# Kernel tuning notes

Measured on AMD Instinct MI355X. Metric: run time of the kernel, lower is better.

Reference implementation:

```python
import jax, jax.numpy as jnp
import numpy as np


def _gru_dir(x, Wih, Whh, bih, bhh):
    # x: (B,T,I) -> (B,T,H); torch GRU equations, h0 = 0
    H = Whh.shape[1]
    pre = x @ Wih.T + bih  # (B,T,3H), input projection hoisted out of scan
    def step(h, p):
        gh = h @ Whh.T + bhh
        pr, pz, pn = jnp.split(p, 3, axis=-1)
        gr, gz, gn = jnp.split(gh, 3, axis=-1)
        r = jax.nn.sigmoid(pr + gr)
        z = jax.nn.sigmoid(pz + gz)
        n = jnp.tanh(pn + r * gn)
        h = (1.0 - z) * n + z * h
        return h, h
    h0 = jnp.zeros((x.shape[0], H), x.dtype)
    _, ys = jax.lax.scan(step, h0, jnp.swapaxes(pre, 0, 1))
    return jnp.swapaxes(ys, 0, 1)


def _gru_bidir(x, Wih, Whh, bih, bhh):
    f = _gru_dir(x, Wih[0], Whh[0], bih[0], bhh[0])
    b = _gru_dir(x[:, ::-1], Wih[1], Whh[1], bih[1], bhh[1])[:, ::-1]
    return jnp.concatenate([f, b], axis=-1)


def _forward(inputs, embed, l_Wih, l_Whh, l_bih, l_bhh, r_Wih, r_Whh, r_bih, r_bhh,
             a_Wih, a_Whh, a_bih, a_bhh, Wc1, Wc2, vc, Wb, Wd, vd, Wm, vm, Ws, vs,
             Wp, vp, Wpred):
    x = embed[inputs]  # (B,T,E)
    hl = _gru_bidir(x, l_Wih, l_Whh, l_bih, l_bhh)  # (B,T,2H)
    hr = _gru_bidir(x, r_Wih, r_Whh, r_bih, r_bhh)  # (B,T,2H)
    # co-attention: score[b,i,j] = vc . tanh(Wc1 hl_j + Wc2 hr_i)
    s = jnp.tanh((hl @ Wc1.T)[:, None, :, :] + (hr @ Wc2.T)[:, :, None, :])  # (B,T,T,H)
    ptc = jax.nn.softmax((s @ vc.T)[..., 0], axis=-1) @ hl
    # bilinear: hr (Wb hl)^T
    sjt = jnp.einsum('bid,bjd->bij', hr, hl @ Wb.T)
    ptb = jax.nn.softmax(sjt, axis=-1) @ hl
    # multiplicative: vd . tanh(Wd (hl_j * hr_i))
    p = hl[:, None, :, :] * hr[:, :, None, :]  # (B,T,T,2H)
    ptd = jax.nn.softmax((jnp.tanh(p @ Wd.T) @ vd.T)[..., 0], axis=-1) @ hl
    # subtractive: vm . tanh(Wm (hl_j - hr_i))
    d = hl[:, None, :, :] - hr[:, :, None, :]  # (B,T,T,2H)
    ptm = jax.nn.softmax((jnp.tanh(d @ Wm.T) @ vm.T)[..., 0], axis=-1) @ hl
    # self-attention on hr: vs . tanh(Ws (hr_j * hr_i))
    ss = hr[:, None, :, :] * hr[:, :, None, :]  # (B,T,T,2H)
    pts = jax.nn.softmax((jnp.tanh(ss @ Ws.T) @ vs.T)[..., 0], axis=-1) @ hr
    agg = jnp.concatenate([hr, pts, ptc, ptd, ptb, ptm], axis=-1)  # (B,T,12H)
    ar = _gru_bidir(agg, a_Wih, a_Whh, a_bih, a_bhh)  # (B,T,2H)
    # pooling of hl
    sj = jax.nn.softmax(jnp.swapaxes(jnp.tanh(hl @ Wp.T) @ vp.T, 1, 2), axis=-1)  # (B,1,T)
    rl = sj @ hl  # (B,1,2H)
    # final attention over aggregation
    sj2 = jax.nn.softmax(jnp.swapaxes((ar @ Wc1.T + rl @ Wc2.T) @ vc.T, 1, 2), axis=-1)  # (B,1,T)
    rr = (sj2 @ ar)[:, 0, :]  # (B,2H)
    return jax.nn.sigmoid(rr @ Wpred.T)  # (B,labels)


def setup_inputs() -> dict:
    B, T, V, E, H, L = 4, 256, 30000, 300, 128, 2
    key = jax.random.key(0)
    ks = jax.random.split(key, 40)
    inp = {}
    inp['inputs'] = jax.random.randint(ks[0], (B, T), 0, V)
    inp['embed'] = jax.random.uniform(ks[1], (V, E), jnp.float32, -0.1, 0.1)
    ki = 2
    for name, isz in [('l', E), ('r', E), ('a', 12 * H)]:
        inp[name + '_Wih'] = jax.random.normal(ks[ki], (2, 3 * H, isz), jnp.float32) * 0.05; ki += 1
        inp[name + '_Whh'] = jax.random.normal(ks[ki], (2, 3 * H, H), jnp.float32) * 0.05; ki += 1
        inp[name + '_bih'] = jnp.zeros((2, 3 * H), jnp.float32)
        inp[name + '_bhh'] = jnp.zeros((2, 3 * H), jnp.float32)
    for n, o, i in [('Wc1', H, 2 * H), ('Wc2', H, 2 * H), ('vc', 1, H), ('Wb', 2 * H, 2 * H),
                    ('Wd', H, 2 * H), ('vd', 1, H), ('Wm', H, 2 * H), ('vm', 1, H),
                    ('Ws', H, 2 * H), ('vs', 1, H), ('Wp', H, 2 * H), ('vp', 1, H),
                    ('Wpred', L, 2 * H)]:
        inp[n] = jax.random.normal(ks[ki], (o, i), jnp.float32) * 0.05; ki += 1
    return inp


def reference(inputs, embed, l_Wih, l_Whh, l_bih, l_bhh, r_Wih, r_Whh, r_bih, r_bhh,
              a_Wih, a_Whh, a_bih, a_bhh, Wc1, Wc2, vc, Wb, Wd, vd, Wm, vm, Ws, vs,
              Wp, vp, Wpred):
    return _forward(inputs, embed, l_Wih, l_Whh, l_bih, l_bhh, r_Wih, r_Whh, r_bih,
                    r_bhh, a_Wih, a_Whh, a_bih, a_bhh, Wc1, Wc2, vc, Wb, Wd, vd, Wm,
                    vm, Ws, vs, Wp, vp, Wpred)
```

## Files before the change

kernel.cpp:

```cpp
#include <hip/hip_runtime.h>


#define DEV static __device__ __forceinline__
#define BAR_LGKM() __asm__ volatile("s_waitcnt lgkmcnt(0)\ns_barrier" ::: "memory")

typedef __attribute__((ext_vector_type(4))) float f32x4;
typedef __attribute__((ext_vector_type(8))) short s16x8;
typedef __attribute__((ext_vector_type(4))) unsigned int u32x4;

constexpr int T = 256, E = 300, EP = 320, H = 128, H2 = 256, H3 = 384, H12 = 1536;
constexpr int M = 1024;
constexpr int STY = 262144;

DEV float b2f(unsigned short h) { return __uint_as_float(((unsigned)h) << 16); }
DEV unsigned short f2b(float f) {
  unsigned u = __float_as_uint(f);
  u += 0x7fff + ((u >> 16) & 1);
  return (unsigned short)(u >> 16);
}
DEV unsigned cvt_pk_bf16(float lo, float hi) {
  unsigned r;
  __asm__("v_cvt_pk_bf16_f32 %0, %1, %2" : "=v"(r) : "v"(lo), "v"(hi));
  return r;
}
DEV float rcp_f(float x) {
  float r;
  __asm__("v_rcp_f32 %0, %1" : "=v"(r) : "v"(x));
  return r;
}
DEV float sigm(float x) { return rcp_f(1.f + __expf(-x)); }
DEV float tanh_f(float x) {
  float e = __expf(2.f * x);
  return __builtin_fmaf(-2.f, rcp_f(e + 1.f), 1.f);
}

DEV s16x8 ldfrag(const unsigned short* p) {
  u32x4 v = *(const u32x4*)p;
  return __builtin_bit_cast(s16x8, v);
}
DEV f32x4 mfma16(s16x8 a, s16x8 b, f32x4 c) {
  return __builtin_amdgcn_mfma_f32_16x16x32_bf16(a, b, c, 0, 0, 0);
}


struct StageArgs {
  const float* cs[9]; unsigned short* cd[9]; int cn[9];
  const int* idx; const float* emb; unsigned short* xhi; unsigned short* xlo;
  const float* lW; const float* rW; unsigned short* wpad;
};

__global__ void k_stage(StageArgs sa) {
  int seg = blockIdx.y;
  int i = blockIdx.x * 256 + threadIdx.x;
  if (seg < 9) {
    if (i < sa.cn[seg]) sa.cd[seg][i] = f2b(sa.cs[seg][i]);
    return;
  }
  if (seg == 9) {
    if (i >= M * EP) return;
    int m = i / EP, e = i - m * EP;
    int r = sa.idx[m];
    float v = (e < E) ? sa.emb[(size_t)r * E + e] : 0.f;
    unsigned short hi = f2b(v);
    sa.xhi[i] = hi;
    sa.xlo[i] = f2b(v - b2f(hi));
    return;
  }
  if (i >= 4 * H3 * EP) return;
  int e = i % EP, n = (i / EP) % H3, uu = i / (EP * H3);
  const float* src = (uu < 2 ? sa.lW : sa.rW) + (size_t)((uu & 1) * H3 + n) * E;
  sa.wpad[i] = (e < E) ? f2b(src[e]) : (unsigned short)0;
}


struct GemmDesc {
  const unsigned short* Ahi; const unsigned short* Alo; const unsigned short* W;
  const float* bias; float* Cf; int N; int K; int tr;
};
struct GemmBatch { GemmDesc d[8]; };

__global__ __launch_bounds__(256) void k_gemm(GemmBatch gb) {
  GemmDesc g = gb.d[blockIdx.z];
  int nb = blockIdx.y * 64;
  if (nb >= g.N) return;
  int mb = blockIdx.x * 64;
  int lane = threadIdx.x & 63, w = threadIdx.x >> 6, quad = lane >> 4, l16 = lane & 15;
  int K = g.K;
  const unsigned short* Ahp = g.Ahi + (size_t)(mb + w * 16 + l16) * K + quad * 8;
  const unsigned short* Alp = g.Alo + (size_t)(mb + w * 16 + l16) * K + quad * 8;
  const unsigned short* Wp = g.W + (size_t)(nb + l16) * K + quad * 8;
  f32x4 acc[4];
  #pragma unroll
  for (int nt = 0; nt < 4; ++nt) acc[nt] = f32x4{0.f, 0.f, 0.f, 0.f};
  for (int k = 0; k < K; k += 32) {
    s16x8 ah = ldfrag(Ahp + k);
    s16x8 al = ldfrag(Alp + k);
    #pragma unroll
    for (int nt = 0; nt < 4; ++nt) {
      s16x8 b = ldfrag(Wp + (size_t)nt * 16 * K + k);
      acc[nt] = mfma16(ah, b, acc[nt]);
      acc[nt] = mfma16(al, b, acc[nt]);
    }
  }
  int mr0 = mb + w * 16 + quad * 4;
  #pragma unroll
  for (int nt = 0; nt < 4; ++nt) {
    int col = nb + nt * 16 + l16;
    float bv = g.bias ? g.bias[col] : 0.f;
    #pragma unroll
    for (int r = 0; r < 4; ++r) {
      if (g.tr)
        g.Cf[(size_t)col * M + (mr0 + r)] = acc[nt][r] + bv;
      else
        g.Cf[(size_t)(mr0 + r) * g.N + col] = acc[nt][r] + bv;
    }
  }
}


struct RecArgs {
  const unsigned short* whh[4];
  const float* pre[4];
  float* outf[4];
  unsigned short* outhi[4];
  unsigned short* outlo[4];
  unsigned short* agghi[4];
  unsigned short* agglo[4];
  const float* bhh[4];
  int colOff[4];
  int dir[4];
};

__global__ __launch_bounds__(512) void k_gru(RecArgs ra) {
  int u = blockIdx.x;
  __shared__ __align__(16) unsigned short hs[2][16 * 136];
  int tid = threadIdx.x, lane = tid & 63, w8 = tid >> 6;
  int quad = lane >> 4, l16 = lane & 15;
  for (int i = tid; i < 2 * 16 * 136; i += 512) ((unsigned short*)hs)[i] = 0;
  const unsigned short* whh = ra.whh[u];
  s16x8 bq[3][4];
  #pragma unroll
  for (int g = 0; g < 3; ++g) {
    int row = g * 128 + w8 * 16 + l16;
    #pragma unroll
    for (int kc = 0; kc < 4; ++kc)
      bq[g][kc] = ldfrag(whh + (size_t)row * H + kc * 32 + quad * 8);
  }
  const float* bhh = ra.bhh[u];
  const float* pre = ra.pre[u];
  float* outf = ra.outf[u];
  unsigned short* outhi = ra.outhi[u];
  unsigned short* outlo = ra.outlo[u];
  unsigned short* agghi = ra.agghi[u];
  unsigned short* agglo = ra.agglo[u];
  int colOff = ra.colOff[u], dir = ra.dir[u];
  int b = ((quad & 1) << 1) | (quad >> 1);
  int d = w8 * 16 + l16;
  float bh_r = bhh[d], bh_z = bhh[d + 128], bh_n = bhh[d + 256];
  float hf = 0.f;
  float ob[8];
  unsigned short obh[8], obl[8];
  int t0 = dir ? (T - 1) : 0;
  const float* pq = pre + (size_t)(b * T + t0) * H3 + d;
  float n_pr = pq[0], n_pz = pq[128], n_pn = pq[256];
  long pst = dir ? -(long)H3 : (long)H3;
  __syncthreads();
  for (int sb = 0; sb < T; sb += 8) {
    #pragma unroll
    for (int ss = 0; ss < 8; ++ss) {
      float pr = n_pr, pz = n_pz, pn = n_pn;
      pq += pst;
      n_pr = pq[0]; n_pz = pq[128]; n_pn = pq[256];
      const unsigned short* hcur = hs[ss & 1];
      unsigned short* hnxt = hs[(ss & 1) ^ 1];
      s16x8 ah[4];
      #pragma unroll
      for (int kc = 0; kc < 4; ++kc)
        ah[kc] = ldfrag(hcur + l16 * 136 + kc * 32 + quad * 8);
      f32x4 accA[3], accB[3];
      #pragma unroll
      for (int g = 0; g < 3; ++g) {
        accA[g] = f32x4{0.f, 0.f, 0.f, 0.f};
        accB[g] = f32x4{0.f, 0.f, 0.f, 0.f};
      }
      #pragma unroll
      for (int g = 0; g < 3; ++g) accA[g] = mfma16(ah[0], bq[g][0], accA[g]);
      #pragma unroll
      for (int g = 0; g < 3; ++g) accB[g] = mfma16(ah[2], bq[g][2], accB[g]);
      #pragma unroll
      for (int g = 0; g < 3; ++g) accA[g] = mfma16(ah[1], bq[g][1], accA[g]);
      #pragma unroll
      for (int g = 0; g < 3; ++g) accB[g] = mfma16(ah[3], bq[g][3], accB[g]);
      float ghv[3];
      #pragma unroll
      for (int g = 0; g < 3; ++g) {
        float x0 = (accA[g][0] + accB[g][0]) + (accA[g][1] + accB[g][1]);
        float x1 = (accA[g][2] + accB[g][2]) + (accA[g][3] + accB[g][3]);
        float y1 = __shfl_xor(x1, 32);
        ghv[g] = (quad >= 2) ? y1 : x0;
      }
      float rg = sigm(pr + ghv[0] + bh_r);
      float zg = sigm(pz + ghv[1] + bh_z);
      float ng = tanh_f(pn + rg * (ghv[2] + bh_n));
      hf = (1.f - zg) * ng + zg * hf;
      unsigned short hi = f2b(hf);
      unsigned short lo = f2b(hf - b2f(hi));
      hnxt[(2 * b) * 136 + d] = hi;
      hnxt[(2 * b + 1) * 136 + d] = lo;
      ob[ss] = hf; obh[ss] = hi; obl[ss] = lo;
      BAR_LGKM();
    }
    #pragma unroll
    for (int qq = 0; qq < 8; ++qq) {
      int sq = sb + qq;
      int tq = dir ? (T - 1 - sq) : sq;
      size_t o = (size_t)(b * T + tq) * H2 + colOff + d;
      outf[o] = ob[qq]; outhi[o] = obh[qq]; outlo[o] = obl[qq];
      if (agghi) {
        size_t a = (size_t)(b * T + tq) * H12 + colOff + d;
        agghi[a] = obh[qq]; agglo[a] = obl[qq];
      }
    }
  }
}


struct ScArgs {
  const unsigned short* Xhi[2];
  const float* Rf; const float* Wt[2]; const float* vt[2];
  float* So[2]; float* So2[2];
  const float *Hc, *Rc, *Hm, *Rm, *HB, *hrf, *vcf, *vmf; float* S;
};

__global__ __launch_bounds__(256, 2) void k_score(ScArgs a) {
  __shared__ __align__(16) unsigned char smem[32768];
  int which = blockIdx.y;
  int bi = blockIdx.x;
  int tid = threadIdx.x;
  if (which == 4) {
    if (bi >= 128) return;
    int b = bi >> 5, i0 = (bi & 31) << 3;
    int gi0 = b * 256 + i0;
    float* rc_l = (float*)smem;
    float* rm_l = rc_l + 1024;
    float* hr_l = rm_l + 1024;
    float* vc_l = hr_l + 2048;
    float* vm_l = vc_l + 128;
    {
      const float4* rc4 = (const float4*)(a.Rc + (size_t)gi0 * 128);
      const float4* rm4 = (const float4*)(a.Rm + (size_t)gi0 * 128);
      ((float4*)rc_l)[tid] = rc4[tid];
      ((float4*)rm_l)[tid] = rm4[tid];
      const float4* hr4 = (const float4*)(a.hrf + (size_t)gi0 * 256);
      ((float4*)hr_l)[tid] = hr4[tid];
      ((float4*)hr_l)[256 + tid] = hr4[256 + tid];
      if (tid < 128) { vc_l[tid] = a.vcf[tid]; vm_l[tid] = a.vmf[tid]; }
    }
    __syncthreads();
    int j = tid;
    size_t cb = (size_t)(b * 256 + j);
    float scq[8], smq[8], sbq[8];
    #pragma unroll
    for (int q = 0; q < 8; ++q) { scq[q] = 0.f; smq[q] = 0.f; sbq[q] = 0.f; }
    for (int k = 0; k < 128; ++k) {
      float hc = a.Hc[(size_t)k * M + cb];
      float hm = a.Hm[(size_t)k * M + cb];
      float vck = vc_l[k], vmk = vm_l[k];
      #pragma unroll
      for (int q = 0; q < 8; ++q) {
        scq[q] += vck * tanh_f(hc + rc_l[q * 128 + k]);
        smq[q] += vmk * tanh_f(hm - rm_l[q * 128 + k]);
      }
    }
    for (int k = 0; k < 256; ++k) {
      float hb = a.HB[(size_t)k * M + cb];
      #pragma unroll
      for (int q = 0; q < 8; ++q) sbq[q] += hb * hr_l[q * 256 + k];
    }
    #pragma unroll
    for (int q = 0; q < 8; ++q) {
      size_t o = (size_t)(gi0 + q) * 256 + j;
      a.S[(size_t)STY * 1 + o] = scq[q];
      a.S[(size_t)STY * 3 + o] = sbq[q];
      a.S[(size_t)STY * 4 + o] = smq[q];
    }
    return;
  }
  int type = which >> 1, khb = which & 1;
  int b = bi >> 8;
  const unsigned short* Xhi = a.Xhi[type];
  const float* W = a.Wt[type] + (size_t)khb * 64 * 256;
  const float* v = a.vt[type] + khb * 64;
  float* Sout = khb ? a.So2[type] : a.So[type];
  unsigned short* w_lds = (unsigned short*)smem;
  int lane = tid & 63, w = tid >> 6, quad = lane >> 4, l16 = lane & 15;
  int d4 = tid & 63, rhi = tid >> 6;
  float4 h4 = ((const float4*)(a.Rf + (size_t)bi * 256))[d4];
  #pragma unroll
  for (int it = 0; it < 16; ++it) {
    int kl = it * 4 + rhi;
    float4 w4 = ((const float4*)(W + (size_t)kl * 256))[d4];
    unsigned lo32 = cvt_pk_bf16(w4.x * h4.x, w4.y * h4.y);
    unsigned hi32 = cvt_pk_bf16(w4.z * h4.z, w4.w * h4.w);
    unsigned long long pk = (unsigned long long)lo32 | ((unsigned long long)hi32 << 32);
    int gphys = ((d4 >> 1) + kl) & 31;
    *(unsigned long long*)(w_lds + (size_t)kl * 256 + gphys * 8 + (d4 & 1) * 4) = pk;
  }
  BAR_LGKM();
  s16x8 afr[4][8];
  #pragma unroll
  for (int c = 0; c < 4; ++c) {
    int krow = c * 16 + l16;
    #pragma unroll
    for (int kc = 0; kc < 8; ++kc) {
      int gp = (kc * 4 + quad + krow) & 31;
      afr[c][kc] = ldfrag(w_lds + (size_t)krow * 256 + gp * 8);
    }
  }
  float vv[4][4];
  #pragma unroll
  for (int c = 0; c < 4; ++c)
    #pragma unroll
    for (int r = 0; r < 4; ++r) vv[c][r] = v[c * 16 + quad * 4 + r];
  #pragma unroll
  for (int jj = 0; jj < 4; ++jj) {
    int jt = w * 4 + jj;
    const unsigned short* Xp = Xhi + (size_t)(b * 256 + jt * 16 + l16) * 256 + quad * 8;
    s16x8 bf[8];
    #pragma unroll
    for (int kc = 0; kc < 8; ++kc) bf[kc] = ldfrag(Xp + kc * 32);
    f32x4 acc[4];
    #pragma unroll
    for (int c = 0; c < 4; ++c) acc[c] = f32x4{0.f, 0.f, 0.f, 0.f};
    #pragma unroll
    for (int kc = 0; kc < 8; ++kc) {
      #pragma unroll
      for (int c = 0; c < 4; ++c) acc[c] = mfma16(afr[c][kc], bf[kc], acc[c]);
    }
    float s = 0.f;
    #pragma unroll
    for (int c = 0; c < 4; ++c)
      #pragma unroll
      for (int r = 0; r < 4; ++r) s += tanh_f(acc[c][r]) * vv[c][r];
    s += __shfl_xor(s, 16);
    s += __shfl_xor(s, 32);
    if (lane < 16) Sout[(size_t)bi * 256 + jt * 16 + l16] = s;
  }
}


__global__ __launch_bounds__(256) void k_wsum(const float* __restrict__ S,
    const float* __restrict__ S2,
    const float* __restrict__ hl_f, const float* __restrict__ hr_f,
    unsigned short* __restrict__ ahi, unsigned short* __restrict__ alo) {
  int it = blockIdx.x, type = blockIdx.y, b = blockIdx.z;
  __shared__ float p_l[8][256];
  __shared__ float red[4];
  int tid = threadIdx.x;
  for (int ii = 0; ii < 8; ++ii) {
    size_t idx = ((size_t)(b * 256 + it * 8 + ii)) * 256 + tid;
    float x = S[(size_t)type * STY + idx];
    if (type == 0) x += S2[idx];
    else if (type == 2) x += S2[(size_t)STY + idx];
    float m = x;
    for (int dl = 32; dl; dl >>= 1) m = fmaxf(m, __shfl_xor(m, dl));
    if ((tid & 63) == 0) red[tid >> 6] = m;
    __syncthreads();
    m = fmaxf(fmaxf(red[0], red[1]), fmaxf(red[2], red[3]));
    __syncthreads();
    float e = __expf(x - m);
    float sum = e;
    for (int dl = 32; dl; dl >>= 1) sum += __shfl_xor(sum, dl);
    if ((tid & 63) == 0) red[tid >> 6] = sum;
    __syncthreads();
    sum = red[0] + red[1] + red[2] + red[3];
    p_l[ii][tid] = e * rcp_f(sum);
    __syncthreads();
  }
  const float* src = (type == 0 ? hr_f : hl_f) + (size_t)b * 256 * 256;
  float acc[8] = {0.f, 0.f, 0.f, 0.f, 0.f, 0.f, 0.f, 0.f};
  for (int j = 0; j < 256; ++j) {
    float hv = src[(size_t)j * 256 + tid];
    #pragma unroll
    for (int ii = 0; ii < 8; ++ii) acc[ii] += p_l[ii][j] * hv;
  }
  int off = 256 * (1 + type);
  #pragma unroll
  for (int ii = 0; ii < 8; ++ii) {
    float vv = acc[ii];
    unsigned short hi = f2b(vv);
    size_t o = (size_t)(b * 256 + it * 8 + ii) * H12 + off + tid;
    ahi[o] = hi;
    alo[o] = f2b(vv - b2f(hi));
  }
}


__global__ __launch_bounds__(256) void k_tail(const float* __restrict__ Hp,
    const float* __restrict__ hl_f, const float* __restrict__ vpf,
    const float* __restrict__ Wc2f, const float* __restrict__ Arc,
    const float* __restrict__ ar_f, const float* __restrict__ vcf,
    const float* __restrict__ Wpredf, float* __restrict__ out) {
  int b = blockIdx.x, tid = threadIdx.x;
  __shared__ float vl[128], wl[256], rvec[256], rlcl[128], red[4];
  if (tid < 128) vl[tid] = vpf[tid];
  __syncthreads();
  const float* hp = Hp + (size_t)(b * 256 + tid) * 128;
  float s = 0.f;
  for (int k = 0; k < 128; ++k) s += vl[k] * tanh_f(hp[k]);
  float m = s;
  for (int dl = 32; dl; dl >>= 1) m = fmaxf(m, __shfl_xor(m, dl));
  if ((tid & 63) == 0) red[tid >> 6] = m;
  __syncthreads();
  m = fmaxf(fmaxf(red[0], red[1]), fmaxf(red[2], red[3]));
  __syncthreads();
  float e = __expf(s - m);
  float sum = e;
  for (int dl = 32; dl; dl >>= 1) sum += __shfl_xor(sum, dl);
  if ((tid & 63) == 0) red[tid >> 6] = sum;
  __syncthreads();
  sum = red[0] + red[1] + red[2] + red[3];
  wl[tid] = e * rcp_f(sum);
  __syncthreads();
  float acc = 0.f;
  for (int t = 0; t < 256; ++t) acc += wl[t] * hl_f[(size_t)(b * 256 + t) * 256 + tid];
  rvec[tid] = acc;
  __syncthreads();
  if (tid < 128) {
    float a2 = 0.f;
    const float* wr = Wc2f + (size_t)tid * 256;
    for (int dk = 0; dk < 256; ++dk) a2 += rvec[dk] * wr[dk];
    rlcl[tid] = a2;
    vl[tid] = vcf[tid];
  }
  __syncthreads();
  const float* ap = Arc + (size_t)(b * 256 + tid) * 128;
  float s2 = 0.f;
  for (int k = 0; k < 128; ++k) s2 += vl[k] * (ap[k] + rlcl[k]);
  m = s2;
  for (int dl = 32; dl; dl >>= 1) m = fmaxf(m, __shfl_xor(m, dl));
  if ((tid & 63) == 0) red[tid >> 6] = m;
  __syncthreads();
  m = fmaxf(fmaxf(red[0], red[1]), fmaxf(red[2], red[3]));
  __syncthreads();
  float e2 = __expf(s2 - m);
  float sum2 = e2;
  for (int dl = 32; dl; dl >>= 1) sum2 += __shfl_xor(sum2, dl);
  if ((tid & 63) == 0) red[tid >> 6] = sum2;
  __syncthreads();
  sum2 = red[0] + red[1] + red[2] + red[3];
  wl[tid] = e2 * rcp_f(sum2);
  __syncthreads();
  float acc2 = 0.f;
  for (int t = 0; t < 256; ++t) acc2 += wl[t] * ar_f[(size_t)(b * 256 + t) * 256 + tid];
  rvec[tid] = acc2;
  __syncthreads();
  if (tid < 2) {
    float o = 0.f;
    const float* wp = Wpredf + (size_t)tid * 256;
    for (int dk = 0; dk < 256; ++dk) o += rvec[dk] * wp[dk];
    out[b * 2 + tid] = sigm(o);
  }
}


extern "C" void kernel_launch(void* const* d_in, const int* in_sizes, int n_in,
                              void* d_out, int out_size, void* d_ws, size_t ws_size,
                              hipStream_t stream) {
  (void)in_sizes; (void)n_in; (void)out_size; (void)ws_size;
  const int* inputs = (const int*)d_in[0];
  const float* embed = (const float*)d_in[1];
  const float* lWih = (const float*)d_in[2];
  const float* lWhh = (const float*)d_in[3];
  const float* lbih = (const float*)d_in[4];
  const float* lbhh = (const float*)d_in[5];
  const float* rWih = (const float*)d_in[6];
  const float* rWhh = (const float*)d_in[7];
  const float* rbih = (const float*)d_in[8];
  const float* rbhh = (const float*)d_in[9];
  const float* aWih = (const float*)d_in[10];
  const float* aWhh = (const float*)d_in[11];
  const float* abih = (const float*)d_in[12];
  const float* abhh = (const float*)d_in[13];
  const float* Wc1 = (const float*)d_in[14];
  const float* Wc2 = (const float*)d_in[15];
  const float* vc  = (const float*)d_in[16];
  const float* Wb  = (const float*)d_in[17];
  const float* Wd  = (const float*)d_in[18];
  const float* vd  = (const float*)d_in[19];
  const float* Wm  = (const float*)d_in[20];
  const float* vmv = (const float*)d_in[21];
  const float* Wsw = (const float*)d_in[22];
  const float* vsv = (const float*)d_in[23];
  const float* Wp  = (const float*)d_in[24];
  const float* vp  = (const float*)d_in[25];
  const float* Wpred = (const float*)d_in[26];

  char* ws = (char*)d_ws;
  size_t off = 0;
  auto alloc = [&](size_t bytes) -> void* {
    void* p = ws + off;
    off += (bytes + 255) & ~(size_t)255;
    return p;
  };
  unsigned short* xhi = (unsigned short*)alloc((size_t)M * EP * 2);
  unsigned short* xlo = (unsigned short*)alloc((size_t)M * EP * 2);
  unsigned short* wpad = (unsigned short*)alloc((size_t)4 * H3 * EP * 2);
  unsigned short* Whh_b = (unsigned short*)alloc((size_t)6 * H3 * H * 2);
  unsigned short* aWih_b = (unsigned short*)alloc((size_t)2 * H3 * H12 * 2);
  unsigned short* Wc1_b = (unsigned short*)alloc((size_t)H * H2 * 2);
  unsigned short* Wc2_b = (unsigned short*)alloc((size_t)H * H2 * 2);
  unsigned short* Wm_b  = (unsigned short*)alloc((size_t)H * H2 * 2);
  unsigned short* Wp_b  = (unsigned short*)alloc((size_t)H * H2 * 2);
  unsigned short* Wb_b  = (unsigned short*)alloc((size_t)H2 * H2 * 2);
  char* region1 = (char*)alloc((size_t)4 * M * H3 * 4);
  float* pre_lr = (float*)region1;
  float* S      = (float*)region1;
  float* pre_a  = (float*)region1;
  float* S2 = (float*)alloc((size_t)2 * STY * 4);
  float* hl_f = (float*)alloc((size_t)M * H2 * 4);
  float* hr_f = (float*)alloc((size_t)M * H2 * 4);
  unsigned short* hl_hi = (unsigned short*)alloc((size_t)M * H2 * 2);
  unsigned short* hl_lo = (unsigned short*)alloc((size_t)M * H2 * 2);
  unsigned short* hr_hi = (unsigned short*)alloc((size_t)M * H2 * 2);
  unsigned short* hr_lo = (unsigned short*)alloc((size_t)M * H2 * 2);
  float* Hc = (float*)alloc((size_t)M * H * 4);
  float* Rc = (float*)alloc((size_t)M * H * 4);
  float* Hm = (float*)alloc((size_t)M * H * 4);
  float* Rm = (float*)alloc((size_t)M * H * 4);
  float* Hp = (float*)alloc((size_t)M * H * 4);
  float* HB = (float*)alloc((size_t)M * H2 * 4);
  unsigned short* agg_hi = (unsigned short*)alloc((size_t)M * H12 * 2);
  unsigned short* agg_lo = (unsigned short*)alloc((size_t)M * H12 * 2);
  float* ar_f = (float*)alloc((size_t)M * H2 * 4);
  unsigned short* ar_hi = (unsigned short*)alloc((size_t)M * H2 * 2);
  unsigned short* ar_lo = (unsigned short*)alloc((size_t)M * H2 * 2);
  float* Arc = (float*)alloc((size_t)M * H * 4);

  StageArgs sa{};
  sa.cs[0] = lWhh;  sa.cd[0] = Whh_b;                 sa.cn[0] = 2 * H3 * H;
  sa.cs[1] = rWhh;  sa.cd[1] = Whh_b + 2 * H3 * H;    sa.cn[1] = 2 * H3 * H;
  sa.cs[2] = aWhh;  sa.cd[2] = Whh_b + 4 * H3 * H;    sa.cn[2] = 2 * H3 * H;
  sa.cs[3] = aWih;  sa.cd[3] = aWih_b;                sa.cn[3] = 2 * H3 * H12;
  sa.cs[4] = Wc1;   sa.cd[4] = Wc1_b;                 sa.cn[4] = H * H2;
  sa.cs[5] = Wc2;   sa.cd[5] = Wc2_b;                 sa.cn[5] = H * H2;
  sa.cs[6] = Wm;    sa.cd[6] = Wm_b;                  sa.cn[6] = H * H2;
  sa.cs[7] = Wp;    sa.cd[7] = Wp_b;                  sa.cn[7] = H * H2;
  sa.cs[8] = Wb;    sa.cd[8] = Wb_b;                  sa.cn[8] = H2 * H2;
  sa.idx = inputs; sa.emb = embed; sa.xhi = xhi; sa.xlo = xlo;
  sa.lW = lWih; sa.rW = rWih; sa.wpad = wpad;
  k_stage<<<dim3((2 * H3 * H12 + 255) / 256, 11), dim3(256), 0, stream>>>(sa);

  GemmBatch ga{};
  const float* biases[4] = { lbih, lbih + H3, rbih, rbih + H3 };
  for (int u = 0; u < 4; ++u)
    ga.d[u] = GemmDesc{ xhi, xlo, wpad + (size_t)u * H3 * EP, biases[u],
                        pre_lr + (size_t)u * M * H3, H3, EP, 0 };
  k_gemm<<<dim3(16, 6, 4), dim3(256), 0, stream>>>(ga);

  RecArgs r1{};
  r1.whh[0] = Whh_b;               r1.whh[1] = Whh_b + H3 * H;
  r1.whh[2] = Whh_b + 2 * H3 * H;  r1.whh[3] = Whh_b + 3 * H3 * H;
  for (int u = 0; u < 4; ++u) r1.pre[u] = pre_lr + (size_t)u * M * H3;
  r1.outf[0] = r1.outf[1] = hl_f; r1.outf[2] = r1.outf[3] = hr_f;
  r1.outhi[0] = r1.outhi[1] = hl_hi; r1.outhi[2] = r1.outhi[3] = hr_hi;
  r1.outlo[0] = r1.outlo[1] = hl_lo; r1.outlo[2] = r1.outlo[3] = hr_lo;
  r1.agghi[0] = r1.agghi[1] = nullptr; r1.agghi[2] = r1.agghi[3] = agg_hi;
  r1.agglo[0] = r1.agglo[1] = nullptr; r1.agglo[2] = r1.agglo[3] = agg_lo;
  r1.bhh[0] = lbhh; r1.bhh[1] = lbhh + H3; r1.bhh[2] = rbhh; r1.bhh[3] = rbhh + H3;
  r1.colOff[0] = 0; r1.colOff[1] = H; r1.colOff[2] = 0; r1.colOff[3] = H;
  r1.dir[0] = 0; r1.dir[1] = 1; r1.dir[2] = 0; r1.dir[3] = 1;
  k_gru<<<dim3(4), dim3(512), 0, stream>>>(r1);

  GemmBatch gbB{};
  gbB.d[0] = GemmDesc{ hl_hi, hl_lo, Wc1_b, nullptr, Hc, H, H2, 1 };
  gbB.d[1] = GemmDesc{ hr_hi, hr_lo, Wc2_b, nullptr, Rc, H, H2, 0 };
  gbB.d[2] = GemmDesc{ hl_hi, hl_lo, Wm_b, nullptr, Hm, H, H2, 1 };
  gbB.d[3] = GemmDesc{ hr_hi, hr_lo, Wm_b, nullptr, Rm, H, H2, 0 };
  gbB.d[4] = GemmDesc{ hl_hi, hl_lo, Wb_b, nullptr, HB, H2, H2, 1 };
  gbB.d[5] = GemmDesc{ hl_hi, hl_lo, Wp_b, nullptr, Hp, H, H2, 0 };
  k_gemm<<<dim3(16, 4, 6), dim3(256), 0, stream>>>(gbB);

  ScArgs sc{};
  sc.Xhi[0] = hl_hi; sc.Wt[0] = Wd;  sc.vt[0] = vd;  sc.So[0] = S + (size_t)2 * STY;
  sc.Xhi[1] = hr_hi; sc.Wt[1] = Wsw; sc.vt[1] = vsv; sc.So[1] = S + (size_t)0 * STY;
  sc.So2[0] = S2 + (size_t)STY;
  sc.So2[1] = S2;
  sc.Rf = hr_f;
  sc.Hc = Hc; sc.Rc = Rc; sc.Hm = Hm; sc.Rm = Rm; sc.HB = HB;
  sc.hrf = hr_f; sc.vcf = vc; sc.vmf = vmv; sc.S = S;
  k_score<<<dim3(M, 5), dim3(256), 0, stream>>>(sc);

  k_wsum<<<dim3(32, 5, 4), dim3(256), 0, stream>>>(S, S2, hl_f, hr_f, agg_hi, agg_lo);

  GemmBatch gc{};
  gc.d[0] = GemmDesc{ agg_hi, agg_lo, aWih_b, abih, pre_a, H3, H12, 0 };
  gc.d[1] = GemmDesc{ agg_hi, agg_lo, aWih_b + (size_t)H3 * H12, abih + H3,
                      pre_a + (size_t)M * H3, H3, H12, 0 };
  k_gemm<<<dim3(16, 6, 2), dim3(256), 0, stream>>>(gc);

  RecArgs r2{};
  r2.whh[0] = Whh_b + 4 * H3 * H; r2.whh[1] = Whh_b + 5 * H3 * H;
  r2.whh[2] = r2.whh[3] = Whh_b + 4 * H3 * H;
  r2.pre[0] = pre_a; r2.pre[1] = pre_a + (size_t)M * H3;
  r2.pre[2] = r2.pre[3] = pre_a;
  r2.outf[0] = r2.outf[1] = r2.outf[2] = r2.outf[3] = ar_f;
  r2.outhi[0] = r2.outhi[1] = r2.outhi[2] = r2.outhi[3] = ar_hi;
  r2.outlo[0] = r2.outlo[1] = r2.outlo[2] = r2.outlo[3] = ar_lo;
  for (int u = 0; u < 4; ++u) { r2.agghi[u] = nullptr; r2.agglo[u] = nullptr; }
  r2.bhh[0] = abhh; r2.bhh[1] = abhh + H3; r2.bhh[2] = r2.bhh[3] = abhh;
  r2.colOff[0] = 0; r2.colOff[1] = H; r2.colOff[2] = r2.colOff[3] = 0;
  r2.dir[0] = 0; r2.dir[1] = 1; r2.dir[2] = r2.dir[3] = 0;
  k_gru<<<dim3(2), dim3(512), 0, stream>>>(r2);

  GemmBatch gd{};
  gd.d[0] = GemmDesc{ ar_hi, ar_lo, Wc1_b, nullptr, Arc, H, H2, 0 };
  k_gemm<<<dim3(16, 2, 1), dim3(256), 0, stream>>>(gd);

  k_tail<<<dim3(4), dim3(256), 0, stream>>>(Hp, hl_f, vp, Wc2, Arc, ar_f, vc, Wpred,
                                            (float*)d_out);
}
```

Baseline: 741.8 us.

## Split score kernel into MFMA and combined-attention kernels; restructure MFMA loop

```diff
diff --git a/kernel.cpp b/kernel.cpp
--- a/kernel.cpp
+++ b/kernel.cpp
@@ -225,74 +225,22 @@
 }
 
 
-struct ScArgs {
+struct ScMMArgs {
   const unsigned short* Xhi[2];
   const float* Rf; const float* Wt[2]; const float* vt[2];
   float* So[2]; float* So2[2];
-  const float *Hc, *Rc, *Hm, *Rm, *HB, *hrf, *vcf, *vmf; float* S;
 };
 
-__global__ __launch_bounds__(256, 2) void k_score(ScArgs a) {
-  __shared__ __align__(16) unsigned char smem[32768];
+__global__ __launch_bounds__(256, 2) void k_scmm(ScMMArgs a) {
+  __shared__ __align__(16) unsigned short w_lds[64 * 256];
   int which = blockIdx.y;
-  int bi = blockIdx.x;
+  int bi = blockIdx.x, b = bi >> 8;
   int tid = threadIdx.x;
-  if (which == 4) {
-    if (bi >= 128) return;
-    int b = bi >> 5, i0 = (bi & 31) << 3;
-    int gi0 = b * 256 + i0;
-    float* rc_l = (float*)smem;
-    float* rm_l = rc_l + 1024;
-    float* hr_l = rm_l + 1024;
-    float* vc_l = hr_l + 2048;
-    float* vm_l = vc_l + 128;
-    {
-      const float4* rc4 = (const float4*)(a.Rc + (size_t)gi0 * 128);
-      const float4* rm4 = (const float4*)(a.Rm + (size_t)gi0 * 128);
-      ((float4*)rc_l)[tid] = rc4[tid];
-      ((float4*)rm_l)[tid] = rm4[tid];
-      const float4* hr4 = (const float4*)(a.hrf + (size_t)gi0 * 256);
-      ((float4*)hr_l)[tid] = hr4[tid];
-      ((float4*)hr_l)[256 + tid] = hr4[256 + tid];
-      if (tid < 128) { vc_l[tid] = a.vcf[tid]; vm_l[tid] = a.vmf[tid]; }
-    }
-    __syncthreads();
-    int j = tid;
-    size_t cb = (size_t)(b * 256 + j);
-    float scq[8], smq[8], sbq[8];
-    #pragma unroll
-    for (int q = 0; q < 8; ++q) { scq[q] = 0.f; smq[q] = 0.f; sbq[q] = 0.f; }
-    for (int k = 0; k < 128; ++k) {
-      float hc = a.Hc[(size_t)k * M + cb];
-      float hm = a.Hm[(size_t)k * M + cb];
-      float vck = vc_l[k], vmk = vm_l[k];
-      #pragma unroll
-      for (int q = 0; q < 8; ++q) {
-        scq[q] += vck * tanh_f(hc + rc_l[q * 128 + k]);
-        smq[q] += vmk * tanh_f(hm - rm_l[q * 128 + k]);
-      }
-    }
-    for (int k = 0; k < 256; ++k) {
-      float hb = a.HB[(size_t)k * M + cb];
-      #pragma unroll
-      for (int q = 0; q < 8; ++q) sbq[q] += hb * hr_l[q * 256 + k];
-    }
-    #pragma unroll
-    for (int q = 0; q < 8; ++q) {
-      size_t o = (size_t)(gi0 + q) * 256 + j;
-      a.S[(size_t)STY * 1 + o] = scq[q];
-      a.S[(size_t)STY * 3 + o] = sbq[q];
-      a.S[(size_t)STY * 4 + o] = smq[q];
-    }
-    return;
-  }
   int type = which >> 1, khb = which & 1;
-  int b = bi >> 8;
   const unsigned short* Xhi = a.Xhi[type];
   const float* W = a.Wt[type] + (size_t)khb * 64 * 256;
   const float* v = a.vt[type] + khb * 64;
   float* Sout = khb ? a.So2[type] : a.So[type];
-  unsigned short* w_lds = (unsigned short*)smem;
   int lane = tid & 63, w = tid >> 6, quad = lane >> 4, l16 = lane & 15;
   int d4 = tid & 63, rhi = tid >> 6;
   float4 h4 = ((const float4*)(a.Rf + (size_t)bi * 256))[d4];
@@ -307,15 +255,31 @@
     *(unsigned long long*)(w_lds + (size_t)kl * 256 + gphys * 8 + (d4 & 1) * 4) = pk;
   }
   BAR_LGKM();
-  s16x8 afr[4][8];
-  #pragma unroll
-  for (int c = 0; c < 4; ++c) {
-    int krow = c * 16 + l16;
-    #pragma unroll
-    for (int kc = 0; kc < 8; ++kc) {
+  f32x4 acc[4][4];
+  #pragma unroll
+  for (int jj = 0; jj < 4; ++jj)
+    #pragma unroll
+    for (int c = 0; c < 4; ++c) acc[jj][c] = f32x4{0.f, 0.f, 0.f, 0.f};
+  const unsigned short* Xp0 =
+      Xhi + (size_t)(b * 256 + w * 4 * 16 + l16) * 256 + quad * 8;
+  #pragma unroll 2
+  for (int kc = 0; kc < 8; ++kc) {
+    s16x8 af[4];
+    #pragma unroll
+    for (int c = 0; c < 4; ++c) {
+      int krow = c * 16 + l16;
       int gp = (kc * 4 + quad + krow) & 31;
-      afr[c][kc] = ldfrag(w_lds + (size_t)krow * 256 + gp * 8);
+      af[c] = ldfrag(w_lds + (size_t)krow * 256 + gp * 8);
     }
+    s16x8 bf[4];
+    #pragma unroll
+    for (int jj = 0; jj < 4; ++jj)
+      bf[jj] = ldfrag(Xp0 + (size_t)jj * 16 * 256 + kc * 32);
+    #pragma unroll
+    for (int jj = 0; jj < 4; ++jj)
+      #pragma unroll
+      for (int c = 0; c < 4; ++c)
+        acc[jj][c] = mfma16(af[c], bf[jj], acc[jj][c]);
   }
   float vv[4][4];
   #pragma unroll
@@ -324,27 +288,69 @@
     for (int r = 0; r < 4; ++r) vv[c][r] = v[c * 16 + quad * 4 + r];
   #pragma unroll
   for (int jj = 0; jj < 4; ++jj) {
-    int jt = w * 4 + jj;
-    const unsigned short* Xp = Xhi + (size_t)(b * 256 + jt * 16 + l16) * 256 + quad * 8;
-    s16x8 bf[8];
-    #pragma unroll
-    for (int kc = 0; kc < 8; ++kc) bf[kc] = ldfrag(Xp + kc * 32);
-    f32x4 acc[4];
-    #pragma unroll
-    for (int c = 0; c < 4; ++c) acc[c] = f32x4{0.f, 0.f, 0.f, 0.f};
-    #pragma unroll
-    for (int kc = 0; kc < 8; ++kc) {
-      #pragma unroll
-      for (int c = 0; c < 4; ++c) acc[c] = mfma16(afr[c][kc], bf[kc], acc[c]);
-    }
     float s = 0.f;
     #pragma unroll
     for (int c = 0; c < 4; ++c)
       #pragma unroll
-      for (int r = 0; r < 4; ++r) s += tanh_f(acc[c][r]) * vv[c][r];
+      for (int r = 0; r < 4; ++r) s += tanh_f(acc[jj][c][r]) * vv[c][r];
     s += __shfl_xor(s, 16);
     s += __shfl_xor(s, 32);
+    int jt = w * 4 + jj;
     if (lane < 16) Sout[(size_t)bi * 256 + jt * 16 + l16] = s;
+  }
+}
+
+
+struct ScCmbArgs {
+  const float *Hc, *Rc, *Hm, *Rm, *HB, *hrf, *vcf, *vmf; float* S;
+};
+
+__global__ __launch_bounds__(256, 2) void k_sccmb(ScCmbArgs a) {
+  int bi = blockIdx.x;
+  int tid = threadIdx.x;
+  __shared__ float rc_l[8 * 128];
+  __shared__ float rm_l[8 * 128];
+  __shared__ float hr_l[8 * 256];
+  __shared__ float vc_l[128], vm_l[128];
+  int b = bi >> 5, i0 = (bi & 31) << 3;
+  int gi0 = b * 256 + i0;
+  {
+    const float4* rc4 = (const float4*)(a.Rc + (size_t)gi0 * 128);
+    const float4* rm4 = (const float4*)(a.Rm + (size_t)gi0 * 128);
+    ((float4*)rc_l)[tid] = rc4[tid];
+    ((float4*)rm_l)[tid] = rm4[tid];
+    const float4* hr4 = (const float4*)(a.hrf + (size_t)gi0 * 256);
+    ((float4*)hr_l)[tid] = hr4[tid];
+    ((float4*)hr_l)[256 + tid] = hr4[256 + tid];
+    if (tid < 128) { vc_l[tid] = a.vcf[tid]; vm_l[tid] = a.vmf[tid]; }
+  }
+  __syncthreads();
+  int j = tid;
+  size_t cb = (size_t)(b * 256 + j);
+  float scq[8], smq[8], sbq[8];
+  #pragma unroll
+  for (int q = 0; q < 8; ++q) { scq[q] = 0.f; smq[q] = 0.f; sbq[q] = 0.f; }
+  for (int k = 0; k < 128; ++k) {
+    float hc = a.Hc[(size_t)k * M + cb];
+    float hm = a.Hm[(size_t)k * M + cb];
+    float vck = vc_l[k], vmk = vm_l[k];
+    #pragma unroll
+    for (int q = 0; q < 8; ++q) {
+      scq[q] += vck * tanh_f(hc + rc_l[q * 128 + k]);
+      smq[q] += vmk * tanh_f(hm - rm_l[q * 128 + k]);
+    }
+  }
+  for (int k = 0; k < 256; ++k) {
+    float hb = a.HB[(size_t)k * M + cb];
+    #pragma unroll
+    for (int q = 0; q < 8; ++q) sbq[q] += hb * hr_l[q * 256 + k];
+  }
+  #pragma unroll
+  for (int q = 0; q < 8; ++q) {
+    size_t o = (size_t)(gi0 + q) * 256 + j;
+    a.S[(size_t)STY * 1 + o] = scq[q];
+    a.S[(size_t)STY * 3 + o] = sbq[q];
+    a.S[(size_t)STY * 4 + o] = smq[q];
   }
 }
 
@@ -581,15 +587,18 @@
   gbB.d[5] = GemmDesc{ hl_hi, hl_lo, Wp_b, nullptr, Hp, H, H2, 0 };
   k_gemm<<<dim3(16, 4, 6), dim3(256), 0, stream>>>(gbB);
 
-  ScArgs sc{};
-  sc.Xhi[0] = hl_hi; sc.Wt[0] = Wd;  sc.vt[0] = vd;  sc.So[0] = S + (size_t)2 * STY;
-  sc.Xhi[1] = hr_hi; sc.Wt[1] = Wsw; sc.vt[1] = vsv; sc.So[1] = S + (size_t)0 * STY;
-  sc.So2[0] = S2 + (size_t)STY;
-  sc.So2[1] = S2;
-  sc.Rf = hr_f;
-  sc.Hc = Hc; sc.Rc = Rc; sc.Hm = Hm; sc.Rm = Rm; sc.HB = HB;
-  sc.hrf = hr_f; sc.vcf = vc; sc.vmf = vmv; sc.S = S;
-  k_score<<<dim3(M, 5), dim3(256), 0, stream>>>(sc);
+  ScMMArgs sm{};
+  sm.Xhi[0] = hl_hi; sm.Wt[0] = Wd;  sm.vt[0] = vd;  sm.So[0] = S + (size_t)2 * STY;
+  sm.Xhi[1] = hr_hi; sm.Wt[1] = Wsw; sm.vt[1] = vsv; sm.So[1] = S + (size_t)0 * STY;
+  sm.So2[0] = S2 + (size_t)STY;
+  sm.So2[1] = S2;
+  sm.Rf = hr_f;
+  k_scmm<<<dim3(M, 4), dim3(256), 0, stream>>>(sm);
+
+  ScCmbArgs scb{};
+  scb.Hc = Hc; scb.Rc = Rc; scb.Hm = Hm; scb.Rm = Rm; scb.HB = HB;
+  scb.hrf = hr_f; scb.vcf = vc; scb.vmf = vmv; scb.S = S;
+  k_sccmb<<<dim3(128), dim3(256), 0, stream>>>(scb);
 
   k_wsum<<<dim3(32, 5, 4), dim3(256), 0, stream>>>(S, S2, hl_f, hr_f, agg_hi, agg_lo);
 
```

Result: no change. 748.4 us (+0.9%).
